# Optimization experiments

Measured on AMD Instinct MI355X. Metric: run time of the kernel, lower is better.

The kernel has to match this reference:

```python
import jax, jax.numpy as jnp
import numpy as np

ALPHA = 8.3  # depth-similarity decay from Depth-aware CNN
K = 3        # kernel size
PAD = 1      # padding (stride=1, dilation=1)


def _patches(x, k, pad):
    """Extract kxk stride-1 patches. x: (B,C,H,W) -> (B,C,k,k,H,W)."""
    B, C, H, W = x.shape
    xp = jnp.pad(x, ((0, 0), (0, 0), (pad, pad), (pad, pad)))
    rows = []
    for i in range(k):
        cols = [xp[:, :, i:i + H, j:j + W] for j in range(k)]
        rows.append(jnp.stack(cols, axis=2))          # (B,C,k,H,W)
    return jnp.stack(rows, axis=2)                     # (B,C,k,k,H,W)


def setup_inputs() -> dict:
    key = jax.random.key(0)
    k1, k2, k3 = jax.random.split(key, 3)
    B, Cin, H, W = 8, 512, 64, 64
    Cout = 64
    x = jax.random.normal(k1, (B, Cin, H, W), dtype=jnp.float32)
    depth = jax.random.uniform(k2, (B, 1, H, W), dtype=jnp.float32)
    stdv = 1.0 / np.sqrt(Cin * K * K)
    weight = jax.random.uniform(k3, (Cout, Cin, K, K), dtype=jnp.float32,
                                minval=-stdv, maxval=stdv)
    return {"input": x, "depth": depth, "weight": weight}


def reference(input, depth, weight):
    # depth-modulated conv: out(p0) = sum_pn w(pn) * x(p0+pn) * exp(-a*|d(p0)-d(p0+pn)|)
    xpat = _patches(input, K, PAD)                 # (B,Cin,K,K,H,W)
    dpat = _patches(depth, K, PAD)                 # (B,1,K,K,H,W)
    d0 = depth[:, :, None, None, :, :]             # center depth (B,1,1,1,H,W)
    gate = jnp.exp(-ALPHA * jnp.abs(d0 - dpat))    # (B,1,K,K,H,W)
    out = jnp.einsum('ocij,bcijhw->bohw', weight, xpat * gate)
    return out
```

## Files before the change

kernel.cpp:

```cpp
#include <hip/hip_runtime.h>
#include <math.h>

#define ALPHA 8.3f
#define XSZ   16896
#define WSZ   36864
#define BUFSZ 53760

typedef short v8s  __attribute__((ext_vector_type(8)));
typedef float v16f __attribute__((ext_vector_type(16)));
typedef float v4f  __attribute__((ext_vector_type(4)));

static __device__ __forceinline__ unsigned short f2bf(float f) {
    unsigned int u = __float_as_uint(f);
    u = (u + 0x7fffu + ((u >> 16) & 1u)) >> 16;
    return (unsigned short)u;
}

static __device__ __forceinline__ void async16(const void* g, void* l) {
    __builtin_amdgcn_global_load_lds(
        (const __attribute__((address_space(1))) unsigned int*)g,
        (__attribute__((address_space(3))) unsigned int*)l, 16, 0, 0);
}

__global__ __launch_bounds__(256) void prep_and_cast(const float* __restrict__ x,
                                                     unsigned short* __restrict__ x2,
                                                     const float* __restrict__ w,
                                                     unsigned short* __restrict__ wt,
                                                     float* __restrict__ zb) {
    __shared__ float st[64][65];
    const int bx  = blockIdx.x;
    const int tid = threadIdx.x;
    if (bx >= 4096) {
        if (bx == 4096) zb[tid] = 0.f;
        const int i = (bx - 4096) * 256 + tid;
        const int j    = i & 7;
        const int lane = (i >> 3) & 63;
        const int F    = i >> 9;
        const int kc   = F & 1;
        const int mt   = (F >> 1) & 1;
        const int tq   = F >> 2;
        const int tap  = tq % 9;
        const int ss   = tq / 9;
        const int o    = mt * 32 + (lane & 31);
        const int cin  = ss * 32 + kc * 16 + (lane >> 5) * 8 + j;
        wt[i] = f2bf(w[(o * 512 + cin) * 9 + tap]);
        return;
    }
    const int cq = bx & 7;
    const int h  = (bx >> 3) & 63;
    const int b  = bx >> 9;
    const float* xb = x + ((size_t)b * 512 + cq * 64) * 4096 + h * 64;
    unsigned short* ob = x2 + (((size_t)b * 64 + h) * 64) * 512 + cq * 64;
#pragma unroll
    for (int i = 0; i < 4; ++i) {
        const int c  = i * 16 + (tid >> 4);
        const int w4 = (tid & 15) * 4;
        const float4 v = *(const float4*)&xb[(size_t)c * 4096 + w4];
        st[c][w4]     = v.x;
        st[c][w4 + 1] = v.y;
        st[c][w4 + 2] = v.z;
        st[c][w4 + 3] = v.w;
    }
    __syncthreads();
#pragma unroll
    for (int j = 0; j < 2; ++j) {
        const int idx = j * 256 + tid;
        const int ww = idx >> 3, k = idx & 7;
        unsigned short t[8];
#pragma unroll
        for (int e = 0; e < 8; ++e) t[e] = f2bf(st[k * 8 + e][ww]);
        uint4 u;
        u.x = t[0] | ((unsigned)t[1] << 16);
        u.y = t[2] | ((unsigned)t[3] << 16);
        u.z = t[4] | ((unsigned)t[5] << 16);
        u.w = t[6] | ((unsigned)t[7] << 16);
        *(uint4*)&ob[(size_t)ww * 512 + k * 8] = u;
    }
}

__global__ __launch_bounds__(384, 2)
void depthconv_v12(const unsigned short* __restrict__ x2,
                   const float* __restrict__ depth,
                   const unsigned short* __restrict__ wt,
                   const float* __restrict__ zbuf,
                   float* __restrict__ out) {
    __shared__ __align__(16) char smem[2 * BUFSZ];

    const int bx   = blockIdx.x;
    const int xcd  = bx & 7;
    const int i0   = bx >> 3;
    const int b    = i0 & 7;
    const int h0   = (xcd * 4 + (i0 >> 3)) * 2;

    const int tid  = threadIdx.x;
    const int wid  = tid >> 6;
    const int lane = tid & 63;
    const int l31  = lane & 31;
    const int half = lane >> 5;
    const int rt   = wid & 1;
    const int di   = wid >> 1;

    const char* xpix = (const char*)(x2 + ((size_t)b * 4096) * 512);

    const char* p0; const char* p1; const char* p2;
#define MKPTR(P, I)                                                              \
    {                                                                            \
        const int g_ = (I) / 264;                                                \
        const int s_ = (I) - g_ * 264;                                           \
        const int r_ = s_ / 66, c_ = s_ - r_ * 66;                               \
        const int hh = h0 - 1 + r_, ww = c_ - 1;                                 \
        P = (hh >= 0 && hh < 64 && ww >= 0 && ww < 64)                           \
                ? xpix + (size_t)(hh * 64 + ww) * 1024 + g_ * 16                 \
                : (const char*)zbuf;                                             \
    }
    MKPTR(p0, tid)
    MKPTR(p1, 384 + tid)
    MKPTR(p2, 768 + tid)
    const char* wsrc = (const char*)wt;

#define ISSUE(BSEL)                                                              \
    {                                                                            \
        char* dst = smem + (BSEL) * BUFSZ;                                       \
        _Pragma("unroll")                                                        \
        for (int k = 0; k < 6; ++k)                                              \
            async16(wsrc + (size_t)(k * 384 + tid) * 16,                         \
                    dst + XSZ + (k * 384 + tid) * 16);                           \
        async16(p0, dst + tid * 16);                                             \
        async16(p1, dst + (384 + tid) * 16);                                     \
        if (tid < 288) async16(p2, dst + (768 + tid) * 16);                      \
        p0 += 64; p1 += 64; p2 += 64; wsrc += WSZ;                               \
    }

    ISSUE(0);

    float gt[2][3];
    {
        const float* dp = depth + (size_t)b * 4096;
        const int hq = h0 + rt;
        const int hn = hq + di - 1;
#pragma unroll
        for (int n = 0; n < 2; ++n) {
            const int wq = n * 32 + l31;
            const float d0 = dp[hq * 64 + wq];
#pragma unroll
            for (int dj = 0; dj < 3; ++dj) {
                const int wn = wq + dj - 1;
                const float dn = (hn >= 0 && hn < 64 && wn >= 0 && wn < 64)
                                     ? dp[hn * 64 + wn] : 0.f;
                gt[n][dj] = __expf(-ALPHA * fabsf(d0 - dn));
            }
        }
    }

    v16f a00[3], a01[3], a10[3], a11[3];
#pragma unroll
    for (int d = 0; d < 3; ++d)
#pragma unroll
        for (int r = 0; r < 16; ++r) { a00[d][r] = 0.f; a01[d][r] = 0.f;
                                       a10[d][r] = 0.f; a11[d][r] = 0.f; }

    const int aOff = XSZ + di * 12288 + lane * 16;
    const int bOff = (half * 264 + (rt + di) * 66 + l31) * 16;

    for (int ss = 0; ss < 16; ++ss) {
        __syncthreads();
        const int cur = ss & 1;
        if (ss < 15) ISSUE(cur ^ 1);
        const char* ba = smem + cur * BUFSZ + aOff;
        const char* bb = smem + cur * BUFSZ + bOff;
#pragma unroll
        for (int dj = 0; dj < 3; ++dj) {
#pragma unroll
            for (int kc = 0; kc < 2; ++kc) {
                const v8s w0 = *(const v8s*)(ba + ((dj * 2 + 0) * 2 + kc) * 1024);
                const v8s w1 = *(const v8s*)(ba + ((dj * 2 + 1) * 2 + kc) * 1024);
                const v8s x0 = *(const v8s*)(bb + kc * 8448 + (0 * 32 + dj) * 16);
                const v8s x1 = *(const v8s*)(bb + kc * 8448 + (1 * 32 + dj) * 16);
                a00[dj] = __builtin_amdgcn_mfma_f32_32x32x16_bf16(w0, x0, a00[dj], 0, 0, 0);
                a01[dj] = __builtin_amdgcn_mfma_f32_32x32x16_bf16(w1, x0, a01[dj], 0, 0, 0);
                a10[dj] = __builtin_amdgcn_mfma_f32_32x32x16_bf16(w0, x1, a10[dj], 0, 0, 0);
                a11[dj] = __builtin_amdgcn_mfma_f32_32x32x16_bf16(w1, x1, a11[dj], 0, 0, 0);
            }
        }
    }

#pragma unroll
    for (int r = 0; r < 16; ++r) {
        a00[0][r] = gt[0][0] * a00[0][r];
        a00[0][r] = fmaf(gt[0][1], a00[1][r], a00[0][r]);
        a00[0][r] = fmaf(gt[0][2], a00[2][r], a00[0][r]);
        a01[0][r] = gt[0][0] * a01[0][r];
        a01[0][r] = fmaf(gt[0][1], a01[1][r], a01[0][r]);
        a01[0][r] = fmaf(gt[0][2], a01[2][r], a01[0][r]);
        a10[0][r] = gt[1][0] * a10[0][r];
        a10[0][r] = fmaf(gt[1][1], a10[1][r], a10[0][r]);
        a10[0][r] = fmaf(gt[1][2], a10[2][r], a10[0][r]);
        a11[0][r] = gt[1][0] * a11[0][r];
        a11[0][r] = fmaf(gt[1][1], a11[1][r], a11[0][r]);
        a11[0][r] = fmaf(gt[1][2], a11[2][r], a11[0][r]);
    }

    __syncthreads();
    float* red = (float*)smem;
    const int rbase = rt * 4096 + lane * 4;
#define EPI_STORE(ACC, N, MT)                                                    \
    _Pragma("unroll")                                                            \
    for (int qd = 0; qd < 4; ++qd) {                                             \
        v4f v; v[0] = ACC[0][qd * 4]; v[1] = ACC[0][qd * 4 + 1];                 \
        v[2] = ACC[0][qd * 4 + 2]; v[3] = ACC[0][qd * 4 + 3];                    \
        *(v4f*)&red[rbase + ((N) * 2 + (MT)) * 1024 + qd * 256] = v;             \
    }
#define EPI_ADD(ACC, N, MT)                                                      \
    _Pragma("unroll")                                                            \
    for (int qd = 0; qd < 4; ++qd) {                                             \
        v4f v = *(const v4f*)&red[rbase + ((N) * 2 + (MT)) * 1024 + qd * 256];   \
        v[0] += ACC[0][qd * 4];     v[1] += ACC[0][qd * 4 + 1];                  \
        v[2] += ACC[0][qd * 4 + 2]; v[3] += ACC[0][qd * 4 + 3];                  \
        *(v4f*)&red[rbase + ((N) * 2 + (MT)) * 1024 + qd * 256] = v;             \
    }
    if (di == 2) {
        EPI_STORE(a00, 0, 0) EPI_STORE(a01, 0, 1) EPI_STORE(a10, 1, 0) EPI_STORE(a11, 1, 1)
    }
    __syncthreads();
    if (di == 1) {
        EPI_ADD(a00, 0, 0) EPI_ADD(a01, 0, 1) EPI_ADD(a10, 1, 0) EPI_ADD(a11, 1, 1)
    }
    __syncthreads();
    if (di == 0) {
        float* ob = out + (size_t)b * 262144 + (h0 + rt) * 64;
#define EPI_OUT(ACC, N, MT)                                                      \
    _Pragma("unroll")                                                            \
    for (int qd = 0; qd < 4; ++qd) {                                             \
        const v4f v = *(const v4f*)&red[rbase + ((N) * 2 + (MT)) * 1024 + qd * 256]; \
        _Pragma("unroll")                                                        \
        for (int j = 0; j < 4; ++j) {                                            \
            const int rg = qd * 4 + j;                                           \
            const int o = (MT) * 32 + (rg & 3) + 8 * (rg >> 2) + 4 * half;       \
            ob[(size_t)o * 4096 + (N) * 32 + l31] = ACC[0][rg] + v[j];           \
        }                                                                        \
    }
        EPI_OUT(a00, 0, 0) EPI_OUT(a01, 0, 1) EPI_OUT(a10, 1, 0) EPI_OUT(a11, 1, 1)
    }
}

extern "C" void kernel_launch(void* const* d_in, const int* in_sizes, int n_in,
                              void* d_out, int out_size, void* d_ws, size_t ws_size,
                              hipStream_t stream) {
    const float* x      = (const float*)d_in[0];
    const float* depth  = (const float*)d_in[1];
    const float* weight = (const float*)d_in[2];
    float* out = (float*)d_out;

    unsigned short* wtb = (unsigned short*)d_ws;
    float* zbuf         = (float*)((char*)d_ws + 786432);
    unsigned short* x2  = (unsigned short*)((char*)d_ws + (1 << 20));

    prep_and_cast<<<5248, 256, 0, stream>>>(x, x2, weight, wtb, zbuf);
    depthconv_v12<<<256, 384, 0, stream>>>(x2, depth, wtb, zbuf, out);
}
```

Measured before the change: 127.8 us.

## Fuse input transpose and bf16 cast into conv kernel's load pipeline

Drops the separate pass that transposed and cast the fp32 input to a bf16 NHWC workspace. The conv kernel now loads fp32 input directly with per-channel strided loads, converts to bf16 in registers, and writes to LDS after the MFMA work of each stage so the loads overlap compute. Weights are still prepped by a smaller kernel. This removes a full read/write pass over the input but adds redundant halo reads in fp32, more register pressure, and a looser launch-bounds occupancy hint.

```diff
diff --git a/kernel.cpp b/kernel.cpp
--- a/kernel.cpp
+++ b/kernel.cpp
@@ -22,67 +22,27 @@
         (__attribute__((address_space(3))) unsigned int*)l, 16, 0, 0);
 }
 
-__global__ __launch_bounds__(256) void prep_and_cast(const float* __restrict__ x,
-                                                     unsigned short* __restrict__ x2,
-                                                     const float* __restrict__ w,
-                                                     unsigned short* __restrict__ wt,
-                                                     float* __restrict__ zb) {
-    __shared__ float st[64][65];
-    const int bx  = blockIdx.x;
-    const int tid = threadIdx.x;
-    if (bx >= 4096) {
-        if (bx == 4096) zb[tid] = 0.f;
-        const int i = (bx - 4096) * 256 + tid;
-        const int j    = i & 7;
-        const int lane = (i >> 3) & 63;
-        const int F    = i >> 9;
-        const int kc   = F & 1;
-        const int mt   = (F >> 1) & 1;
-        const int tq   = F >> 2;
-        const int tap  = tq % 9;
-        const int ss   = tq / 9;
-        const int o    = mt * 32 + (lane & 31);
-        const int cin  = ss * 32 + kc * 16 + (lane >> 5) * 8 + j;
-        wt[i] = f2bf(w[(o * 512 + cin) * 9 + tap]);
-        return;
-    }
-    const int cq = bx & 7;
-    const int h  = (bx >> 3) & 63;
-    const int b  = bx >> 9;
-    const float* xb = x + ((size_t)b * 512 + cq * 64) * 4096 + h * 64;
-    unsigned short* ob = x2 + (((size_t)b * 64 + h) * 64) * 512 + cq * 64;
-#pragma unroll
-    for (int i = 0; i < 4; ++i) {
-        const int c  = i * 16 + (tid >> 4);
-        const int w4 = (tid & 15) * 4;
-        const float4 v = *(const float4*)&xb[(size_t)c * 4096 + w4];
-        st[c][w4]     = v.x;
-        st[c][w4 + 1] = v.y;
-        st[c][w4 + 2] = v.z;
-        st[c][w4 + 3] = v.w;
-    }
-    __syncthreads();
-#pragma unroll
-    for (int j = 0; j < 2; ++j) {
-        const int idx = j * 256 + tid;
-        const int ww = idx >> 3, k = idx & 7;
-        unsigned short t[8];
-#pragma unroll
-        for (int e = 0; e < 8; ++e) t[e] = f2bf(st[k * 8 + e][ww]);
-        uint4 u;
-        u.x = t[0] | ((unsigned)t[1] << 16);
-        u.y = t[2] | ((unsigned)t[3] << 16);
-        u.z = t[4] | ((unsigned)t[5] << 16);
-        u.w = t[6] | ((unsigned)t[7] << 16);
-        *(uint4*)&ob[(size_t)ww * 512 + k * 8] = u;
-    }
-}
-
-__global__ __launch_bounds__(384, 2)
-void depthconv_v12(const unsigned short* __restrict__ x2,
+__global__ __launch_bounds__(256) void prep_weights(const float* __restrict__ w,
+                                                    unsigned short* __restrict__ wt) {
+    const int i = blockIdx.x * 256 + threadIdx.x;
+    if (i >= 294912) return;
+    const int j    = i & 7;
+    const int lane = (i >> 3) & 63;
+    const int F    = i >> 9;
+    const int kc   = F & 1;
+    const int mt   = (F >> 1) & 1;
+    const int tq   = F >> 2;
+    const int tap  = tq % 9;
+    const int ss   = tq / 9;
+    const int o    = mt * 32 + (lane & 31);
+    const int cin  = ss * 32 + kc * 16 + (lane >> 5) * 8 + j;
+    wt[i] = f2bf(w[(o * 512 + cin) * 9 + tap]);
+}
+
+__global__ __launch_bounds__(384)
+void depthconv_v15(const float* __restrict__ x,
                    const float* __restrict__ depth,
                    const unsigned short* __restrict__ wt,
-                   const float* __restrict__ zbuf,
                    float* __restrict__ out) {
     __shared__ __align__(16) char smem[2 * BUFSZ];
 
@@ -100,38 +60,57 @@
     const int rt   = wid & 1;
     const int di   = wid >> 1;
 
-    const char* xpix = (const char*)(x2 + ((size_t)b * 4096) * 512);
-
-    const char* p0; const char* p1; const char* p2;
-#define MKPTR(P, I)                                                              \
+    const float* xb = x + (size_t)b * 2097152;
+    const float* xsrc[3];
+    int  goff[3];
+    bool gval[3], gact[3];
+#pragma unroll
+    for (int it = 0; it < 3; ++it) {
+        const int g_i = it * 384 + tid;
+        const bool act = (g_i < 1056);
+        const int p_ = g_i / 264;
+        const int s_ = g_i - p_ * 264;
+        const int r_ = s_ / 66, c_ = s_ - r_ * 66;
+        const int hh = h0 - 1 + r_, ww = c_ - 1;
+        const bool val = act && hh >= 0 && hh < 64 && ww >= 0 && ww < 64;
+        gact[it] = act;
+        gval[it] = val;
+        goff[it] = g_i * 16;
+        xsrc[it] = val ? (xb + (size_t)(p_ * 8) * 4096 + hh * 64 + ww) : xb;
+    }
+
+#define XLOAD(SS, V)                                                             \
     {                                                                            \
-        const int g_ = (I) / 264;                                                \
-        const int s_ = (I) - g_ * 264;                                           \
-        const int r_ = s_ / 66, c_ = s_ - r_ * 66;                               \
-        const int hh = h0 - 1 + r_, ww = c_ - 1;                                 \
-        P = (hh >= 0 && hh < 64 && ww >= 0 && ww < 64)                           \
-                ? xpix + (size_t)(hh * 64 + ww) * 1024 + g_ * 16                 \
-                : (const char*)zbuf;                                             \
-    }
-    MKPTR(p0, tid)
-    MKPTR(p1, 384 + tid)
-    MKPTR(p2, 768 + tid)
-    const char* wsrc = (const char*)wt;
-
-#define ISSUE(BSEL)                                                              \
+        const size_t adv = (size_t)(SS) * 131072;       \
+        _Pragma("unroll")                                                        \
+        for (int it = 0; it < 3; ++it)                                           \
+            _Pragma("unroll")                                                    \
+            for (int e = 0; e < 8; ++e)                                          \
+                V[it][e] = gval[it] ? xsrc[it][adv + (size_t)e * 4096] : 0.f;    \
+    }
+#define XWRITE(V, BSEL)                                                          \
     {                                                                            \
-        char* dst = smem + (BSEL) * BUFSZ;                                       \
+        char* dx = smem + (BSEL) * BUFSZ;                                        \
+        _Pragma("unroll")                                                        \
+        for (int it = 0; it < 3; ++it)                                           \
+            if (gact[it]) {                                                      \
+                uint4 u;                                                         \
+                u.x = f2bf(V[it][0]) | ((unsigned)f2bf(V[it][1]) << 16);         \
+                u.y = f2bf(V[it][2]) | ((unsigned)f2bf(V[it][3]) << 16);         \
+                u.z = f2bf(V[it][4]) | ((unsigned)f2bf(V[it][5]) << 16);         \
+                u.w = f2bf(V[it][6]) | ((unsigned)f2bf(V[it][7]) << 16);         \
+                *(uint4*)(dx + goff[it]) = u;                                    \
+            }                                                                    \
+    }
+#define WISSUE(SS, BSEL)                                                         \
+    {                                                                            \
+        char* dw = smem + (BSEL) * BUFSZ + XSZ;                                  \
+        const char* ws = (const char*)wt + (size_t)(SS) * WSZ;                   \
         _Pragma("unroll")                                                        \
         for (int k = 0; k < 6; ++k)                                              \
-            async16(wsrc + (size_t)(k * 384 + tid) * 16,                         \
-                    dst + XSZ + (k * 384 + tid) * 16);                           \
-        async16(p0, dst + tid * 16);                                             \
-        async16(p1, dst + (384 + tid) * 16);                                     \
-        if (tid < 288) async16(p2, dst + (768 + tid) * 16);                      \
-        p0 += 64; p1 += 64; p2 += 64; wsrc += WSZ;                               \
-    }
-
-    ISSUE(0);
+            async16(ws + (size_t)(k * 384 + tid) * 16,                           \
+                    dw + (k * 384 + tid) * 16);                                  \
+    }
 
     float gt[2][3];
     {
@@ -162,10 +141,19 @@
     const int aOff = XSZ + di * 12288 + lane * 16;
     const int bOff = (half * 264 + (rt + di) * 66 + l31) * 16;
 
+    float v[3][8];
+    WISSUE(0, 0);
+    XLOAD(0, v);
+    XWRITE(v, 0);
+
     for (int ss = 0; ss < 16; ++ss) {
         __syncthreads();
         const int cur = ss & 1;
-        if (ss < 15) ISSUE(cur ^ 1);
+        const int nxt = cur ^ 1;
+        if (ss < 15) {
+            WISSUE(ss + 1, nxt);
+            XLOAD(ss + 1, v);
+        }
         const char* ba = smem + cur * BUFSZ + aOff;
         const char* bb = smem + cur * BUFSZ + bOff;
 #pragma unroll
@@ -182,6 +170,7 @@
                 a11[dj] = __builtin_amdgcn_mfma_f32_32x32x16_bf16(w1, x1, a11[dj], 0, 0, 0);
             }
         }
+        if (ss < 15) XWRITE(v, nxt);
     }
 
 #pragma unroll
@@ -206,17 +195,17 @@
 #define EPI_STORE(ACC, N, MT)                                                    \
     _Pragma("unroll")                                                            \
     for (int qd = 0; qd < 4; ++qd) {                                             \
-        v4f v; v[0] = ACC[0][qd * 4]; v[1] = ACC[0][qd * 4 + 1];                 \
-        v[2] = ACC[0][qd * 4 + 2]; v[3] = ACC[0][qd * 4 + 3];                    \
-        *(v4f*)&red[rbase + ((N) * 2 + (MT)) * 1024 + qd * 256] = v;             \
+        v4f vv; vv[0] = ACC[0][qd * 4]; vv[1] = ACC[0][qd * 4 + 1];              \
+        vv[2] = ACC[0][qd * 4 + 2]; vv[3] = ACC[0][qd * 4 + 3];                  \
+        *(v4f*)&red[rbase + ((N) * 2 + (MT)) * 1024 + qd * 256] = vv;            \
     }
 #define EPI_ADD(ACC, N, MT)                                                      \
     _Pragma("unroll")                                                            \
     for (int qd = 0; qd < 4; ++qd) {                                             \
-        v4f v = *(const v4f*)&red[rbase + ((N) * 2 + (MT)) * 1024 + qd * 256];   \
-        v[0] += ACC[0][qd * 4];     v[1] += ACC[0][qd * 4 + 1];                  \
-        v[2] += ACC[0][qd * 4 + 2]; v[3] += ACC[0][qd * 4 + 3];                  \
-        *(v4f*)&red[rbase + ((N) * 2 + (MT)) * 1024 + qd * 256] = v;             \
+        v4f vv = *(const v4f*)&red[rbase + ((N) * 2 + (MT)) * 1024 + qd * 256];  \
+        vv[0] += ACC[0][qd * 4];     vv[1] += ACC[0][qd * 4 + 1];                \
+        vv[2] += ACC[0][qd * 4 + 2]; vv[3] += ACC[0][qd * 4 + 3];                \
+        *(v4f*)&red[rbase + ((N) * 2 + (MT)) * 1024 + qd * 256] = vv;            \
     }
     if (di == 2) {
         EPI_STORE(a00, 0, 0) EPI_STORE(a01, 0, 1) EPI_STORE(a10, 1, 0) EPI_STORE(a11, 1, 1)
@@ -231,12 +220,12 @@
 #define EPI_OUT(ACC, N, MT)                                                      \
     _Pragma("unroll")                                                            \
     for (int qd = 0; qd < 4; ++qd) {                                             \
-        const v4f v = *(const v4f*)&red[rbase + ((N) * 2 + (MT)) * 1024 + qd * 256]; \
+        const v4f vv = *(const v4f*)&red[rbase + ((N) * 2 + (MT)) * 1024 + qd * 256]; \
         _Pragma("unroll")                                                        \
         for (int j = 0; j < 4; ++j) {                                            \
             const int rg = qd * 4 + j;                                           \
             const int o = (MT) * 32 + (rg & 3) + 8 * (rg >> 2) + 4 * half;       \
-            ob[(size_t)o * 4096 + (N) * 32 + l31] = ACC[0][rg] + v[j];           \
+            ob[(size_t)o * 4096 + (N) * 32 + l31] = ACC[0][rg] + vv[j];          \
         }                                                                        \
     }
         EPI_OUT(a00, 0, 0) EPI_OUT(a01, 0, 1) EPI_OUT(a10, 1, 0) EPI_OUT(a11, 1, 1)
@@ -252,9 +241,7 @@
     float* out = (float*)d_out;
 
     unsigned short* wtb = (unsigned short*)d_ws;
-    float* zbuf         = (float*)((char*)d_ws + 786432);
-    unsigned short* x2  = (unsigned short*)((char*)d_ws + (1 << 20));
-
-    prep_and_cast<<<5248, 256, 0, stream>>>(x, x2, weight, wtb, zbuf);
-    depthconv_v12<<<256, 384, 0, stream>>>(x2, depth, wtb, zbuf, out);
-}
+
+    prep_weights<<<1152, 256, 0, stream>>>(weight, wtb);
+    depthconv_v15<<<256, 384, 0, stream>>>(x, depth, wtb, out);
+}
```

Result: slower. 133.0 us (+4.1%).
